# Kernel tuning notes

Hardware: AMD Instinct MI355X
Metric: run time of the kernel (lower is better)

## Reference

```python
import jax, jax.numpy as jnp
import numpy as np

B, T, C, H = 4, 2048, 1024, 16
HD = C // H  # head dim = 64


def setup_inputs() -> dict:
    key = jax.random.key(0)
    ks = jax.random.split(key, 5)
    s = 1.0 / np.sqrt(C)
    return {
        "x": jax.random.normal(ks[0], (B, T, C), jnp.float32),
        "Wk": jax.random.normal(ks[1], (C, C), jnp.float32) * s,
        "bk": jnp.zeros((C,), jnp.float32),
        "Wq": jax.random.normal(ks[2], (C, C), jnp.float32) * s,
        "bq": jnp.zeros((C,), jnp.float32),
        "Wv": jax.random.normal(ks[3], (C, C), jnp.float32) * s,
        "bv": jnp.zeros((C,), jnp.float32),
        "Wp": jax.random.normal(ks[4], (C, C), jnp.float32) * s,
        "bp": jnp.zeros((C,), jnp.float32),
    }


def reference(x, Wk, bk, Wq, bq, Wv, bv, Wp, bp):
    # Linear(in, out): y = x @ W.T + b  (W stored as [out, in], torch convention)
    k = (x @ Wk.T + bk).reshape(B, T, H, HD).transpose(0, 2, 1, 3)  # [B,H,T,HD]
    q = (x @ Wq.T + bq).reshape(B, T, H, HD).transpose(0, 2, 1, 3)
    v = (x @ Wv.T + bv).reshape(B, T, H, HD).transpose(0, 2, 1, 3)
    scale = 1.0 / np.sqrt(HD)
    att = jnp.einsum("bhqd,bhkd->bhqk", q, k) * scale  # [B,H,T,T]
    causal = jnp.tril(jnp.ones((T, T), bool))
    att = jnp.where(causal[None, None, :, :], att, -jnp.inf)
    att = jax.nn.softmax(att, axis=-1)
    y = jnp.einsum("bhqk,bhkd->bhqd", att, v)  # [B,H,T,HD]
    y = y.transpose(0, 2, 1, 3).reshape(B, T, C)
    return y @ Wp.T + bp
```

## Files before the change

### kernel.cpp

```cpp
#include <hip/hip_runtime.h>
#include <hip/hip_bf16.h>
#include <cmath>

#define Tt 2048
#define Cc 1024
#define Hh 16
#define HDd 64

typedef __attribute__((ext_vector_type(8))) short short8;
typedef __attribute__((ext_vector_type(4))) float f32x4;

#define ASYNC16(gp, lp)                                       \
    __builtin_amdgcn_global_load_lds(                         \
        (const __attribute__((address_space(1))) void*)(gp),  \
        (__attribute__((address_space(3))) void*)(lp), 16, 0, 0)

__device__ __forceinline__ unsigned short f32_bf16(float f) {
    unsigned u = __float_as_uint(f);
    u += 0x7FFF + ((u >> 16) & 1);
    return (unsigned short)(u >> 16);
}
__device__ __forceinline__ unsigned short f32_bf16_rn(float f) {
    return (unsigned short)((__float_as_uint(f) + 0x8000u) >> 16);
}
__device__ __forceinline__ float fast_exp2(float x) {
#if __has_builtin(__builtin_amdgcn_exp2f)
    return __builtin_amdgcn_exp2f(x);
#else
    return exp2f(x);
#endif
}

__global__ __launch_bounds__(256) void cvt_all(
    const float* __restrict__ x, const float* __restrict__ a,
    const float* __restrict__ b, const float* __restrict__ c,
    const float* __restrict__ d, unsigned short* __restrict__ ox,
    unsigned short* __restrict__ oa, unsigned short* __restrict__ ob,
    unsigned short* __restrict__ oc, unsigned short* __restrict__ od) {
    const int id = blockIdx.x * 256 + threadIdx.x;
    const float* src; unsigned short* dst; int sub;
    if (id < 2097152) {
        src = x; dst = ox; sub = id;
    } else {
        const int wi = id - 2097152;
        const int which = wi >> 18;
        sub = wi & 262143;
        if (which == 0)      { src = a; dst = oa; }
        else if (which == 1) { src = b; dst = ob; }
        else if (which == 2) { src = c; dst = oc; }
        else                 { src = d; dst = od; }
    }
    float4 v = ((const float4*)src)[sub];
    ushort4 o;
    o.x = f32_bf16(v.x); o.y = f32_bf16(v.y);
    o.z = f32_bf16(v.z); o.w = f32_bf16(v.w);
    ((ushort4*)dst)[sub] = o;
}

__global__ __launch_bounds__(512, 2) void gemm_qkv8(
    const unsigned short* __restrict__ A,
    const unsigned short* __restrict__ Wcat,
    const float* __restrict__ bq, const float* __restrict__ bk,
    const float* __restrict__ bv,
    unsigned short* __restrict__ qout, unsigned short* __restrict__ kout,
    unsigned short* __restrict__ vout) {
    extern __shared__ unsigned short lds[];

    const int tid  = threadIdx.x;
    const int wid  = tid >> 6;
    const int lane = tid & 63;
    const int quad = lane >> 4;
    const int lr   = lane & 15;
    const int wr   = wid >> 2;
    const int wc   = wid & 3;

    const int id   = blockIdx.y * 12 + blockIdx.x;
    const int xcd  = id & 7;
    const int rank = id >> 3;
    const int ls   = rank >> 4;
    const int w    = rank & 15;
    const int sID  = ls * 8 + xcd;
    const int by   = (sID / 3) * 4 + (w >> 2);
    const int bx   = (sID % 3) * 4 + (w & 3);
    const int bm0  = by * 256;
    const int bn0  = bx * 256;

    const int srow  = wid * 8 + (lane >> 3);
    const int scol  = ((lane & 7) ^ (lane >> 3)) * 8;
    const int sldso = wid * 512;

    const int a_r   = wr * 64 + lr;
    const int b_r   = wc * 32 + lr;
    const int slot0 = (quad ^ (lr & 7)) * 8;
    const int slot1 = ((quad ^ 4) ^ (lr & 7)) * 8;

    f32x4 acc[8][4];
    const f32x4 zero = {0.f, 0.f, 0.f, 0.f};
#pragma unroll
    for (int i = 0; i < 8; ++i)
#pragma unroll
        for (int j = 0; j < 4; ++j) acc[i][j] = zero;

    short8 areg[4][2];
    short8 breg[2][2][2];

#define STG(S, BUF, REG, GB, GROW)                                          \
    do {                                                                    \
        if ((S) < 16) {                                                     \
            unsigned short* lb = lds + ((BUF) * 4 + (REG)) * 8192 + sldso;  \
            const unsigned short* gp =                                      \
                (GB) + (size_t)((GROW) + srow) * Cc + (S) * 64 + scol;      \
            ASYNC16(gp, lb);                                                \
            ASYNC16(gp + (size_t)64 * Cc, lb + 4096);                       \
        }                                                                   \
    } while (0)

#define LDA(mh)                                                             \
    do {                                                                    \
        const unsigned short* ab = bufb + (mh) * 8192;                      \
        _Pragma("unroll") for (int mf = 0; mf < 4; ++mf) {                  \
            areg[mf][0] = *(const short8*)(ab + (a_r + mf * 16) * 64 + slot0); \
            areg[mf][1] = *(const short8*)(ab + (a_r + mf * 16) * 64 + slot1); \
        }                                                                   \
    } while (0)

#define LDB(nh)                                                             \
    do {                                                                    \
        const unsigned short* bb = bufb + (2 + (nh)) * 8192;                \
        _Pragma("unroll") for (int nf = 0; nf < 2; ++nf) {                  \
            breg[nh][nf][0] = *(const short8*)(bb + (b_r + nf * 16) * 64 + slot0); \
            breg[nh][nf][1] = *(const short8*)(bb + (b_r + nf * 16) * 64 + slot1); \
        }                                                                   \
    } while (0)

#define MFMA_PHASE(mh, nh)                                                  \
    _Pragma("unroll") for (int mf = 0; mf < 4; ++mf)                        \
    _Pragma("unroll") for (int nf = 0; nf < 2; ++nf) {                      \
        acc[(mh)*4+mf][(nh)*2+nf] = __builtin_amdgcn_mfma_f32_16x16x32_bf16( \
            areg[mf][0], breg[nh][nf][0], acc[(mh)*4+mf][(nh)*2+nf], 0,0,0); \
        acc[(mh)*4+mf][(nh)*2+nf] = __builtin_amdgcn_mfma_f32_16x16x32_bf16( \
            areg[mf][1], breg[nh][nf][1], acc[(mh)*4+mf][(nh)*2+nf], 0,0,0); \
    }

#define TILE(T, BC, WN)                                                     \
    {                                                                       \
        const unsigned short* bufb = lds + (BC) * 32768;                    \
        LDA(0);                                                             \
        LDB(0);                                                             \
        STG((T) + 1, (BC) ^ 1, 1, A, bm0 + 128);                            \
        __builtin_amdgcn_s_barrier();                                       \
        asm volatile("s_waitcnt lgkmcnt(0)" ::: "memory");                  \
        __builtin_amdgcn_s_setprio(1);                                      \
        MFMA_PHASE(0, 0);                                                   \
        __builtin_amdgcn_s_setprio(0);                                      \
        __builtin_amdgcn_s_barrier();                                       \
        LDB(1);                                                             \
        STG((T) + 1, (BC) ^ 1, 3, Wcat, bn0 + 128);                         \
        __builtin_amdgcn_s_barrier();                                       \
        asm volatile("s_waitcnt lgkmcnt(0)" ::: "memory");                  \
        __builtin_amdgcn_s_setprio(1);                                      \
        MFMA_PHASE(0, 1);                                                   \
        __builtin_amdgcn_s_setprio(0);                                      \
        __builtin_amdgcn_s_barrier();                                       \
        LDA(1);                                                             \
        STG((T) + 2, (BC), 0, A, bm0);                                      \
        __builtin_amdgcn_s_barrier();                                       \
        asm volatile("s_waitcnt lgkmcnt(0)" ::: "memory");                  \
        __builtin_amdgcn_s_setprio(1);                                      \
        MFMA_PHASE(1, 0);                                                   \
        __builtin_amdgcn_s_setprio(0);                                      \
        __builtin_amdgcn_s_barrier();                                       \
        STG((T) + 2, (BC), 2, Wcat, bn0);                                   \
        __builtin_amdgcn_s_barrier();                                       \
        __builtin_amdgcn_s_setprio(1);                                      \
        MFMA_PHASE(1, 1);                                                   \
        __builtin_amdgcn_s_setprio(0);                                      \
        asm volatile("s_waitcnt vmcnt(" #WN ")" ::: "memory");              \
        __builtin_amdgcn_s_barrier();                                       \
    }

    STG(0, 0, 0, A, bm0);
    STG(0, 0, 1, A, bm0 + 128);
    STG(0, 0, 2, Wcat, bn0);
    STG(0, 0, 3, Wcat, bn0 + 128);
    STG(1, 1, 0, A, bm0);
    STG(1, 1, 2, Wcat, bn0);
    asm volatile("s_waitcnt vmcnt(4)" ::: "memory");
    __builtin_amdgcn_s_barrier();

    for (int t2 = 0; t2 < 7; ++t2) {
        const int T0 = t2 * 2;
        TILE(T0, 0, 4);
        TILE(T0 + 1, 1, 4);
    }
    TILE(14, 0, 0);
    TILE(15, 1, 0);

#undef TILE
#undef MFMA_PHASE
#undef LDB
#undef LDA
#undef STG

    const int which = bn0 >> 10;
    const float* bias = (which == 0) ? bq : (which == 1) ? bk : bv;
    unsigned short* outp = (which == 0) ? qout : (which == 1) ? kout : vout;
    const float scale = (which == 0) ? 0.1803368801111204f : 1.0f;
    const bool vmode = (which == 2);
    const int nb = bn0 & 1023;

#pragma unroll
    for (int nh = 0; nh < 2; ++nh)
#pragma unroll
        for (int nf = 0; nf < 2; ++nf) {
            const int nl = nb + nh * 128 + wc * 32 + nf * 16 + lr;
            const float bvv = bias[nl];
            const int h = nl >> 6, hd = nl & 63;
#pragma unroll
            for (int mh = 0; mh < 2; ++mh)
#pragma unroll
                for (int mf = 0; mf < 4; ++mf) {
                    const f32x4 a = acc[mh * 4 + mf][nh * 2 + nf];
                    const int m0 = bm0 + mh * 128 + wr * 64 + mf * 16 + quad * 4;
                    const int b = m0 >> 11, t0 = m0 & 2047;
                    if (vmode) {
                        ushort4 pk;
                        pk.x = f32_bf16_rn(a[0] + bvv);
                        pk.y = f32_bf16_rn(a[1] + bvv);
                        pk.z = f32_bf16_rn(a[2] + bvv);
                        pk.w = f32_bf16_rn(a[3] + bvv);
                        *(ushort4*)(outp + (((size_t)(b * Hh + h)) * HDd + hd) * Tt + t0) = pk;
                    } else {
#pragma unroll
                        for (int r = 0; r < 4; ++r) {
                            outp[(((size_t)(b * Hh + h)) * Tt + t0 + r) * HDd + hd] =
                                f32_bf16_rn((a[r] + bvv) * scale);
                        }
                    }
                }
        }
}

__global__ __launch_bounds__(512, 2) void gemm_proj8(
    const unsigned short* __restrict__ A,
    const unsigned short* __restrict__ W,
    const float* __restrict__ bias,
    float* __restrict__ out) {
    extern __shared__ unsigned short lds[];

    const int tid  = threadIdx.x;
    const int wid  = tid >> 6;
    const int lane = tid & 63;
    const int quad = lane >> 4;
    const int lr   = lane & 15;
    const int wr   = wid >> 2;
    const int wc   = wid & 3;

    const int id   = blockIdx.y * 8 + blockIdx.x;
    const int xcd  = id & 7;
    const int rank = id >> 3;
    const int by   = xcd * 4 + (rank >> 3);
    const int bx   = rank & 7;
    const int bm0  = by * 256;
    const int bn0  = bx * 128;

    const int srow  = wid * 8 + (lane >> 3);
    const int scol  = ((lane & 7) ^ (lane >> 3)) * 8;
    const int sldso = wid * 512;

    const int a_r   = wr * 64 + lr;
    const int b_r2  = (wc & 1) * 32 + lr;
    const int breg_off = 16384 + (wc >> 1) * 4096;
    const int slot0 = (quad ^ (lr & 7)) * 8;
    const int slot1 = ((quad ^ 4) ^ (lr & 7)) * 8;

    f32x4 acc[8][2];
    const f32x4 zero = {0.f, 0.f, 0.f, 0.f};
#pragma unroll
    for (int i = 0; i < 8; ++i)
#pragma unroll
        for (int j = 0; j < 2; ++j) acc[i][j] = zero;

    short8 areg[4][2];
    short8 breg[2][2];

#define STGA(S, BUF, REG_OFF, GROW)                                         \
    do {                                                                    \
        if ((S) < 16) {                                                     \
            unsigned short* lb = lds + (BUF) * 24576 + (REG_OFF) + sldso;   \
            const unsigned short* gp =                                      \
                A + (size_t)(bm0 + (GROW) + srow) * Cc + (S) * 64 + scol;   \
            ASYNC16(gp, lb);                                                \
            ASYNC16(gp + (size_t)64 * Cc, lb + 4096);                       \
        }                                                                   \
    } while (0)

#define STGB(S, BUF, REG_OFF, NROW)                                         \
    do {                                                                    \
        if ((S) < 16) {                                                     \
            unsigned short* lb = lds + (BUF) * 24576 + (REG_OFF) + sldso;   \
            const unsigned short* gp =                                      \
                W + (size_t)(bn0 + (NROW) + srow) * Cc + (S) * 64 + scol;   \
            ASYNC16(gp, lb);                                                \
        }                                                                   \
    } while (0)

#define LDA_P(mh)                                                           \
    do {                                                                    \
        const unsigned short* ab = bufb + (mh) * 8192;                      \
        _Pragma("unroll") for (int mf = 0; mf < 4; ++mf) {                  \
            areg[mf][0] = *(const short8*)(ab + (a_r + mf * 16) * 64 + slot0); \
            areg[mf][1] = *(const short8*)(ab + (a_r + mf * 16) * 64 + slot1); \
        }                                                                   \
    } while (0)

#define LDB_P                                                               \
    do {                                                                    \
        const unsigned short* bb = bufb + breg_off;                         \
        _Pragma("unroll") for (int nf = 0; nf < 2; ++nf) {                  \
            breg[nf][0] = *(const short8*)(bb + (b_r2 + nf * 16) * 64 + slot0); \
            breg[nf][1] = *(const short8*)(bb + (b_r2 + nf * 16) * 64 + slot1); \
        }                                                                   \
    } while (0)

#define MFMA_P(mh)                                                          \
    _Pragma("unroll") for (int mf = 0; mf < 4; ++mf)                        \
    _Pragma("unroll") for (int nf = 0; nf < 2; ++nf) {                      \
        acc[(mh)*4+mf][nf] = __builtin_amdgcn_mfma_f32_16x16x32_bf16(       \
            areg[mf][0], breg[nf][0], acc[(mh)*4+mf][nf], 0, 0, 0);         \
        acc[(mh)*4+mf][nf] = __builtin_amdgcn_mfma_f32_16x16x32_bf16(       \
            areg[mf][1], breg[nf][1], acc[(mh)*4+mf][nf], 0, 0, 0);         \
    }

#define TILE_P(T, BC, WN)                                                   \
    {                                                                       \
        const unsigned short* bufb = lds + (BC) * 24576;                    \
        LDA_P(0);                                                           \
        LDB_P;                                                              \
        STGA((T) + 1, (BC) ^ 1, 8192, 128);                                 \
        STGB((T) + 1, (BC) ^ 1, 20480, 64);                                 \
        __builtin_amdgcn_s_barrier();                                       \
        asm volatile("s_waitcnt lgkmcnt(0)" ::: "memory");                  \
        __builtin_amdgcn_s_setprio(1);                                      \
        MFMA_P(0);                                                          \
        __builtin_amdgcn_s_setprio(0);                                      \
        __builtin_amdgcn_s_barrier();                                       \
        LDA_P(1);                                                           \
        STGA((T) + 2, (BC), 0, 0);                                          \
        STGB((T) + 2, (BC), 16384, 0);                                      \
        __builtin_amdgcn_s_barrier();                                       \
        asm volatile("s_waitcnt lgkmcnt(0)" ::: "memory");                  \
        __builtin_amdgcn_s_setprio(1);                                      \
        MFMA_P(1);                                                          \
        __builtin_amdgcn_s_setprio(0);                                      \
        asm volatile("s_waitcnt vmcnt(" #WN ")" ::: "memory");              \
        __builtin_amdgcn_s_barrier();                                       \
    }

    STGA(0, 0, 0, 0);
    STGA(0, 0, 8192, 128);
    STGB(0, 0, 16384, 0);
    STGB(0, 0, 20480, 64);
    STGA(1, 1, 0, 0);
    STGB(1, 1, 16384, 0);
    asm volatile("s_waitcnt vmcnt(3)" ::: "memory");
    __builtin_amdgcn_s_barrier();

    for (int t2 = 0; t2 < 7; ++t2) {
        const int T0 = t2 * 2;
        TILE_P(T0, 0, 3);
        TILE_P(T0 + 1, 1, 3);
    }
    TILE_P(14, 0, 0);
    TILE_P(15, 1, 0);

#undef TILE_P
#undef MFMA_P
#undef LDB_P
#undef LDA_P
#undef STGB
#undef STGA

#pragma unroll
    for (int nf = 0; nf < 2; ++nf) {
        const int n = bn0 + wc * 32 + nf * 16 + lr;
        const float bvv = bias[n];
#pragma unroll
        for (int mh = 0; mh < 2; ++mh)
#pragma unroll
            for (int mf = 0; mf < 4; ++mf) {
                const f32x4 a = acc[mh * 4 + mf][nf];
                const int m0 = bm0 + mh * 128 + wr * 64 + mf * 16 + quad * 4;
#pragma unroll
                for (int r = 0; r < 4; ++r)
                    out[(size_t)(m0 + r) * Cc + n] = a[r] + bvv;
            }
    }
}

__global__ __launch_bounds__(256, 4) void attn(const unsigned short* __restrict__ q,
                                               const unsigned short* __restrict__ k,
                                               const unsigned short* __restrict__ vt,
                                               unsigned short* __restrict__ y) {
    __shared__ unsigned short sK[2][64 * 64];
    __shared__ unsigned short sV[2][64 * 64];
    __shared__ unsigned short sP[4][16 * 64];

    const int tid  = threadIdx.x;
    const int wid  = tid >> 6;
    const int lane = tid & 63;
    const int quad = lane >> 4;
    const int lr   = lane & 15;

    const int bh = blockIdx.x;
    const int qx = blockIdx.y;
    const size_t headq = (size_t)bh * Tt * HDd;
    const unsigned short* kg = k + headq;
    const unsigned short* vg = vt + headq;
    const int b = bh >> 4, h = bh & 15;

    const int g_r = lane >> 3;
    const int g_c = ((lane & 7) ^ g_r) * 8;
    const unsigned short* kst = kg + (size_t)(wid * 16 + g_r) * HDd + g_c;
    const unsigned short* vst = vg + (size_t)(wid * 16 + g_r) * Tt + g_c;
    unsigned short* dK0 = sK[0] + wid * 1024;
    unsigned short* dK1 = sK[1] + wid * 1024;
    unsigned short* dV0 = sV[0] + wid * 1024;
    unsigned short* dV1 = sV[1] + wid * 1024;

#define STAGE_KV(BUF, KB)                                                   \
    do {                                                                    \
        unsigned short* dK = (BUF) ? dK1 : dK0;                             \
        unsigned short* dV = (BUF) ? dV1 : dV0;                             \
        ASYNC16(kst + (size_t)(KB) * HDd,       dK);                        \
        ASYNC16(kst + (size_t)((KB) + 8) * HDd, dK + 512);                  \
        ASYNC16(vst + (KB),                     dV);                        \
        ASYNC16(vst + (size_t)8 * Tt + (KB),    dV + 512);                  \
    } while (0)

    const int fr_off = lr * 64 + ((quad ^ (lr & 7)) * 8);
    const int hq8 = (((lr >> 3) ^ ((quad & 1) << 2)) * 8);
    const int pwb = quad * 256 + (lr & 7);
    unsigned short* sPw = sP[wid];

    const f32x4 zero = {0.f, 0.f, 0.f, 0.f};

    for (int pass = 0; pass < 2; ++pass) {
        const int qt = pass ? (31 - qx) : qx;
        const int qb = qt * 64;
        const int ntiles = qt + 1;

        const unsigned short* qp = q + headq + (size_t)(qb + wid * 16 + lr) * HDd;
        const short8 qf0 = *(const short8*)(qp + quad * 8);
        const short8 qf1 = *(const short8*)(qp + 32 + quad * 8);

        f32x4 o[4];
        float l_run[4];
#pragma unroll
        for (int i = 0; i < 4; i++) { o[i] = zero; l_run[i] = 0.f; }

        STAGE_KV(0, 0);
        __syncthreads();

        for (int kt = 0; kt < ntiles; ++kt) {
            const int cur = kt & 1;
            if (kt + 1 < ntiles) STAGE_KV(cur ^ 1, (kt + 1) * 64);

            const unsigned short* bK = sK[cur];
            const unsigned short* bV = sV[cur];

            short8 kf[4][2];
#pragma unroll
            for (int nt = 0; nt < 4; nt++) {
                kf[nt][0] = *(const short8*)(bK + nt * 1024 + fr_off);
                kf[nt][1] = *(const short8*)(bK + nt * 1024 + (fr_off ^ 32));
            }

            f32x4 sc[4];
            __builtin_amdgcn_s_setprio(1);
#pragma unroll
            for (int nt = 0; nt < 4; nt++) {
                f32x4 a = __builtin_amdgcn_mfma_f32_16x16x32_bf16(qf0, kf[nt][0], zero, 0, 0, 0);
                sc[nt]  = __builtin_amdgcn_mfma_f32_16x16x32_bf16(qf1, kf[nt][1], a, 0, 0, 0);
            }
            __builtin_amdgcn_s_setprio(0);

            short8 vf[4][2];
#pragma unroll
            for (int nt = 0; nt < 4; nt++) {
                vf[nt][0] = *(const short8*)(bV + nt * 1024 + fr_off);
                vf[nt][1] = *(const short8*)(bV + nt * 1024 + (fr_off ^ 32));
            }

            if (kt == qt) {
#pragma unroll
                for (int nt = 0; nt < 4; nt++)
#pragma unroll
                    for (int r = 0; r < 4; r++)
                        sc[nt][r] = (nt * 16 + lr <= wid * 16 + quad * 4 + r)
                                        ? sc[nt][r] : -INFINITY;
            }

#pragma unroll
            for (int nt = 0; nt < 4; nt++)
#pragma unroll
                for (int r = 0; r < 4; r++) {
                    const float p = fast_exp2(sc[nt][r]);
                    l_run[r] += p;
                    sPw[pwb + r * 64 + ((nt * 16 ^ r * 8) ^ hq8)] = f32_bf16_rn(p);
                }

            const short8 pa0 = *(const short8*)(sPw + fr_off);
            const short8 pa1 = *(const short8*)(sPw + (fr_off ^ 32));

            __builtin_amdgcn_s_setprio(1);
#pragma unroll
            for (int nt = 0; nt < 4; nt++) {
                o[nt] = __builtin_amdgcn_mfma_f32_16x16x32_bf16(pa0, vf[nt][0], o[nt], 0, 0, 0);
                o[nt] = __builtin_amdgcn_mfma_f32_16x16x32_bf16(pa1, vf[nt][1], o[nt], 0, 0, 0);
            }
            __builtin_amdgcn_s_setprio(0);

            __syncthreads();
        }

#pragma unroll
        for (int r = 0; r < 4; r++) {
            float ls = l_run[r];
            ls += __shfl_xor(ls, 1);
            ls += __shfl_xor(ls, 2);
            ls += __shfl_xor(ls, 4);
            ls += __shfl_xor(ls, 8);
            const float inv = 1.0f / ls;
            const int t = qb + wid * 16 + quad * 4 + r;
#pragma unroll
            for (int nt = 0; nt < 4; nt++) {
                const int dim = nt * 16 + lr;
                y[((size_t)(b * Tt + t)) * Cc + h * HDd + dim] =
                    f32_bf16_rn(o[nt][r] * inv);
            }
        }
    }
#undef STAGE_KV
}

extern "C" void kernel_launch(void* const* d_in, const int* in_sizes, int n_in,
                              void* d_out, int out_size, void* d_ws, size_t ws_size,
                              hipStream_t stream) {
    const float* x  = (const float*)d_in[0];
    const float* Wk = (const float*)d_in[1];
    const float* bk = (const float*)d_in[2];
    const float* Wq = (const float*)d_in[3];
    const float* bq = (const float*)d_in[4];
    const float* Wv = (const float*)d_in[5];
    const float* bv = (const float*)d_in[6];
    const float* Wp = (const float*)d_in[7];
    const float* bp = (const float*)d_in[8];
    float* out = (float*)d_out;

    char* ws = (char*)d_ws;
    size_t off = 0;
    auto alloc = [&](size_t bytes) { char* p = ws + off; off += bytes; return p; };
    const size_t MK = (size_t)8192 * 1024;
    const size_t NK = (size_t)1024 * 1024;
    unsigned short* xb   = (unsigned short*)alloc(MK * 2);
    unsigned short* Wcat = (unsigned short*)alloc(3 * NK * 2);
    unsigned short* Wqb  = Wcat;
    unsigned short* Wkb  = Wcat + NK;
    unsigned short* Wvb  = Wcat + 2 * NK;
    unsigned short* Wpb  = (unsigned short*)alloc(NK * 2);
    unsigned short* qh   = (unsigned short*)alloc(MK * 2);
    unsigned short* kh   = (unsigned short*)alloc(MK * 2);
    unsigned short* vth  = (unsigned short*)alloc(MK * 2);
    unsigned short* ya   = (unsigned short*)alloc(MK * 2);

    static bool lds_attr_set = false;
    if (!lds_attr_set) {
        (void)hipFuncSetAttribute((const void*)gemm_qkv8,
                                  hipFuncAttributeMaxDynamicSharedMemorySize,
                                  131072);
        (void)hipFuncSetAttribute((const void*)gemm_proj8,
                                  hipFuncAttributeMaxDynamicSharedMemorySize,
                                  98304);
        lds_attr_set = true;
    }

    cvt_all<<<12288, 256, 0, stream>>>(x, Wq, Wk, Wv, Wp, xb, Wqb, Wkb, Wvb, Wpb);

    gemm_qkv8<<<dim3(12, 32), 512, 131072, stream>>>(xb, Wcat, bq, bk, bv, qh, kh, vth);

    attn<<<dim3(64, 16), 256, 0, stream>>>(qh, kh, vth, ya);

    gemm_proj8<<<dim3(8, 32), 512, 98304, stream>>>(ya, Wpb, bp, out);
}
```

Baseline: 247.0 us.

## Split fused QKV GEMM into QK GEMM and separate 256x128-tile V GEMM

```diff
diff --git a/kernel.cpp b/kernel.cpp
--- a/kernel.cpp
+++ b/kernel.cpp
@@ -74,14 +74,11 @@
     const int wr   = wid >> 2;
     const int wc   = wid & 3;
 
-    const int id   = blockIdx.y * 12 + blockIdx.x;
+    const int id   = blockIdx.y * 8 + blockIdx.x;
     const int xcd  = id & 7;
     const int rank = id >> 3;
-    const int ls   = rank >> 4;
-    const int w    = rank & 15;
-    const int sID  = ls * 8 + xcd;
-    const int by   = (sID / 3) * 4 + (w >> 2);
-    const int bx   = (sID % 3) * 4 + (w & 3);
+    const int by   = xcd * 4 + (rank >> 3);
+    const int bx   = rank & 7;
     const int bm0  = by * 256;
     const int bn0  = bx * 256;
 
@@ -203,11 +200,11 @@
 #undef STG
 
     const int which = bn0 >> 10;
-    const float* bias = (which == 0) ? bq : (which == 1) ? bk : bv;
-    unsigned short* outp = (which == 0) ? qout : (which == 1) ? kout : vout;
+    const float* bias = (which == 0) ? bq : bk;
+    unsigned short* outp = (which == 0) ? qout : kout;
     const float scale = (which == 0) ? 0.1803368801111204f : 1.0f;
-    const bool vmode = (which == 2);
     const int nb = bn0 & 1023;
+    (void)bv; (void)vout;
 
 #pragma unroll
     for (int nh = 0; nh < 2; ++nh)
@@ -223,22 +220,175 @@
                     const f32x4 a = acc[mh * 4 + mf][nh * 2 + nf];
                     const int m0 = bm0 + mh * 128 + wr * 64 + mf * 16 + quad * 4;
                     const int b = m0 >> 11, t0 = m0 & 2047;
-                    if (vmode) {
-                        ushort4 pk;
-                        pk.x = f32_bf16_rn(a[0] + bvv);
-                        pk.y = f32_bf16_rn(a[1] + bvv);
-                        pk.z = f32_bf16_rn(a[2] + bvv);
-                        pk.w = f32_bf16_rn(a[3] + bvv);
-                        *(ushort4*)(outp + (((size_t)(b * Hh + h)) * HDd + hd) * Tt + t0) = pk;
-                    } else {
-#pragma unroll
-                        for (int r = 0; r < 4; ++r) {
-                            outp[(((size_t)(b * Hh + h)) * Tt + t0 + r) * HDd + hd] =
-                                f32_bf16_rn((a[r] + bvv) * scale);
-                        }
+#pragma unroll
+                    for (int r = 0; r < 4; ++r) {
+                        outp[(((size_t)(b * Hh + h)) * Tt + t0 + r) * HDd + hd] =
+                            f32_bf16_rn((a[r] + bvv) * scale);
                     }
                 }
         }
+}
+
+__global__ __launch_bounds__(512, 2) void gemm_v8(
+    const unsigned short* __restrict__ A,
+    const unsigned short* __restrict__ Wcat,
+    const float* __restrict__ bv,
+    unsigned short* __restrict__ vout) {
+    extern __shared__ unsigned short lds[];
+
+    const int tid  = threadIdx.x;
+    const int wid  = tid >> 6;
+    const int lane = tid & 63;
+    const int quad = lane >> 4;
+    const int lr   = lane & 15;
+    const int wr   = wid >> 2;
+    const int wc   = wid & 3;
+
+    const int id   = blockIdx.y * 8 + blockIdx.x;
+    const int xcd  = id & 7;
+    const int rank = id >> 3;
+    const int by   = xcd * 4 + (rank >> 3);
+    const int bx   = rank & 7;
+    const int bm0  = by * 256;
+    const int wrow0 = 2048 + bx * 128;
+
+    const int srow  = wid * 8 + (lane >> 3);
+    const int scol  = ((lane & 7) ^ (lane >> 3)) * 8;
+    const int sldso = wid * 512;
+
+    const int a_r   = wr * 64 + lr;
+    const int b_r2  = (wc & 1) * 32 + lr;
+    const int breg_off = 16384 + (wc >> 1) * 4096;
+    const int slot0 = (quad ^ (lr & 7)) * 8;
+    const int slot1 = ((quad ^ 4) ^ (lr & 7)) * 8;
+
+    f32x4 acc[8][2];
+    const f32x4 zero = {0.f, 0.f, 0.f, 0.f};
+#pragma unroll
+    for (int i = 0; i < 8; ++i)
+#pragma unroll
+        for (int j = 0; j < 2; ++j) acc[i][j] = zero;
+
+    short8 areg[4][2];
+    short8 breg[2][2];
+
+#define STGAV(S, BUF, REG_OFF, GROW)                                        \
+    do {                                                                    \
+        if ((S) < 16) {                                                     \
+            unsigned short* lb = lds + (BUF) * 24576 + (REG_OFF) + sldso;   \
+            const unsigned short* gp =                                      \
+                A + (size_t)(bm0 + (GROW) + srow) * Cc + (S) * 64 + scol;   \
+            ASYNC16(gp, lb);                                                \
+            ASYNC16(gp + (size_t)64 * Cc, lb + 4096);                       \
+        }                                                                   \
+    } while (0)
+
+#define STGBV(S, BUF, REG_OFF, NROW)                                        \
+    do {                                                                    \
+        if ((S) < 16) {                                                     \
+            unsigned short* lb = lds + (BUF) * 24576 + (REG_OFF) + sldso;   \
+            const unsigned short* gp =                                      \
+                Wcat + (size_t)(wrow0 + (NROW) + srow) * Cc + (S) * 64 + scol; \
+            ASYNC16(gp, lb);                                                \
+        }                                                                   \
+    } while (0)
+
+#define LDA_V(mh)                                                           \
+    do {                                                                    \
+        const unsigned short* ab = bufb + (mh) * 8192;                      \
+        _Pragma("unroll") for (int mf = 0; mf < 4; ++mf) {                  \
+            areg[mf][0] = *(const short8*)(ab + (a_r + mf * 16) * 64 + slot0); \
+            areg[mf][1] = *(const short8*)(ab + (a_r + mf * 16) * 64 + slot1); \
+        }                                                                   \
+    } while (0)
+
+#define LDB_V                                                               \
+    do {                                                                    \
+        const unsigned short* bb = bufb + breg_off;                         \
+        _Pragma("unroll") for (int nf = 0; nf < 2; ++nf) {                  \
+            breg[nf][0] = *(const short8*)(bb + (b_r2 + nf * 16) * 64 + slot0); \
+            breg[nf][1] = *(const short8*)(bb + (b_r2 + nf * 16) * 64 + slot1); \
+        }                                                                   \
+    } while (0)
+
+#define MFMA_V(mh)                                                          \
+    _Pragma("unroll") for (int mf = 0; mf < 4; ++mf)                        \
+    _Pragma("unroll") for (int nf = 0; nf < 2; ++nf) {                      \
+        acc[(mh)*4+mf][nf] = __builtin_amdgcn_mfma_f32_16x16x32_bf16(       \
+            areg[mf][0], breg[nf][0], acc[(mh)*4+mf][nf], 0, 0, 0);         \
+        acc[(mh)*4+mf][nf] = __builtin_amdgcn_mfma_f32_16x16x32_bf16(       \
+            areg[mf][1], breg[nf][1], acc[(mh)*4+mf][nf], 0, 0, 0);         \
+    }
+
+#define TILE_V(T, BC, WN)                                                   \
+    {                                                                       \
+        const unsigned short* bufb = lds + (BC) * 24576;                    \
+        LDA_V(0);                                                           \
+        LDB_V;                                                              \
+        STGAV((T) + 1, (BC) ^ 1, 8192, 128);                                \
+        STGBV((T) + 1, (BC) ^ 1, 20480, 64);                                \
+        __builtin_amdgcn_s_barrier();                                       \
+        asm volatile("s_waitcnt lgkmcnt(0)" ::: "memory");                  \
+        __builtin_amdgcn_s_setprio(1);                                      \
+        MFMA_V(0);                                                          \
+        __builtin_amdgcn_s_setprio(0);                                      \
+        __builtin_amdgcn_s_barrier();                                       \
+        LDA_V(1);                                                           \
+        STGAV((T) + 2, (BC), 0, 0);                                         \
+        STGBV((T) + 2, (BC), 16384, 0);                                     \
+        __builtin_amdgcn_s_barrier();                                       \
+        asm volatile("s_waitcnt lgkmcnt(0)" ::: "memory");                  \
+        __builtin_amdgcn_s_setprio(1);                                      \
+        MFMA_V(1);                                                          \
+        __builtin_amdgcn_s_setprio(0);                                      \
+        asm volatile("s_waitcnt vmcnt(" #WN ")" ::: "memory");              \
+        __builtin_amdgcn_s_barrier();                                       \
+    }
+
+    STGAV(0, 0, 0, 0);
+    STGAV(0, 0, 8192, 128);
+    STGBV(0, 0, 16384, 0);
+    STGBV(0, 0, 20480, 64);
+    STGAV(1, 1, 0, 0);
+    STGBV(1, 1, 16384, 0);
+    asm volatile("s_waitcnt vmcnt(3)" ::: "memory");
+    __builtin_amdgcn_s_barrier();
+
+    for (int t2 = 0; t2 < 7; ++t2) {
+        const int T0 = t2 * 2;
+        TILE_V(T0, 0, 3);
+        TILE_V(T0 + 1, 1, 3);
+    }
+    TILE_V(14, 0, 0);
+    TILE_V(15, 1, 0);
+
+#undef TILE_V
+#undef MFMA_V
+#undef LDB_V
+#undef LDA_V
+#undef STGBV
+#undef STGAV
+
+#pragma unroll
+    for (int nf = 0; nf < 2; ++nf) {
+        const int nl = (wrow0 - 2048) + wc * 32 + nf * 16 + lr;
+        const float bvv = bv[nl];
+        const int h = nl >> 6, hd = nl & 63;
+#pragma unroll
+        for (int mh = 0; mh < 2; ++mh)
+#pragma unroll
+            for (int mf = 0; mf < 4; ++mf) {
+                const f32x4 a = acc[mh * 4 + mf][nf];
+                const int m0 = bm0 + mh * 128 + wr * 64 + mf * 16 + quad * 4;
+                const int b = m0 >> 11, t0 = m0 & 2047;
+                ushort4 pk;
+                pk.x = f32_bf16_rn(a[0] + bvv);
+                pk.y = f32_bf16_rn(a[1] + bvv);
+                pk.z = f32_bf16_rn(a[2] + bvv);
+                pk.w = f32_bf16_rn(a[3] + bvv);
+                *(ushort4*)(vout + (((size_t)(b * Hh + h)) * HDd + hd) * Tt + t0) = pk;
+            }
+    }
 }
 
 __global__ __launch_bounds__(512, 2) void gemm_proj8(
@@ -579,6 +729,9 @@
         (void)hipFuncSetAttribute((const void*)gemm_qkv8,
                                   hipFuncAttributeMaxDynamicSharedMemorySize,
                                   131072);
+        (void)hipFuncSetAttribute((const void*)gemm_v8,
+                                  hipFuncAttributeMaxDynamicSharedMemorySize,
+                                  98304);
         (void)hipFuncSetAttribute((const void*)gemm_proj8,
                                   hipFuncAttributeMaxDynamicSharedMemorySize,
                                   98304);
@@ -587,7 +740,8 @@
 
     cvt_all<<<12288, 256, 0, stream>>>(x, Wq, Wk, Wv, Wp, xb, Wqb, Wkb, Wvb, Wpb);
 
-    gemm_qkv8<<<dim3(12, 32), 512, 131072, stream>>>(xb, Wcat, bq, bk, bv, qh, kh, vth);
+    gemm_qkv8<<<dim3(8, 32), 512, 131072, stream>>>(xb, Wcat, bq, bk, bv, qh, kh, vth);
+    gemm_v8<<<dim3(8, 32), 512, 98304, stream>>>(xb, Wcat, bv, vth);
 
     attn<<<dim3(64, 16), 256, 0, stream>>>(qh, kh, vth, ya);
 
```

Result: no change. 243.4 us (-1.5%).
